# Performance work log

Measured on AMD Instinct MI355X. Metric: run time of the kernel, lower is better.

Reference implementation:

```python
import jax, jax.numpy as jnp
import numpy as np
from jax import lax

RATIO = 0.25
K = 16
EPS = 1e-5
B, N, CX, COUT, CAUX = 16, 4096, 64, 128, 32


def _fps(p, m):
    # Farthest point sampling on one cloud p:(N,3); deterministic start at index 0.
    mind = jnp.sum((p - p[0]) ** 2, axis=-1)  # (N,) min sq-dist to selected set
    def step(mind, _):
        nxt = jnp.argmax(mind)
        d = jnp.sum((p - p[nxt]) ** 2, axis=-1)
        return jnp.minimum(mind, d), nxt
    _, rest = lax.scan(step, mind, None, length=m - 1)
    return jnp.concatenate([jnp.zeros((1,), jnp.int32), rest.astype(jnp.int32)])


def setup_inputs() -> dict:
    key = jax.random.key(0)
    k1, k2, k3, k4, k5, k6 = jax.random.split(key, 6)
    P = B * N
    x = jax.random.normal(k1, (P, CX), jnp.float32)
    pos = jax.random.normal(k2, (P, 3), jnp.float32)
    batch = jnp.repeat(jnp.arange(B, dtype=jnp.int32), N)  # equal-size clouds
    aux = jax.random.normal(k3, (P, CAUX), jnp.float32)
    # MLP params: Linear(CX->COUT) + BatchNorm affine
    W = jax.random.normal(k4, (CX, COUT), jnp.float32) * (1.0 / np.sqrt(CX))
    b = jax.random.normal(k5, (COUT,), jnp.float32) * 0.02
    gamma = jnp.ones((COUT,), jnp.float32) + 0.1 * jax.random.normal(k6, (COUT,), jnp.float32)
    beta = jnp.zeros((COUT,), jnp.float32)
    return {"x": x, "pos": pos, "batch": batch, "aux": aux,
            "W": W, "b": b, "gamma": gamma, "beta": beta}


def reference(x, pos, batch, aux, W, b, gamma, beta):
    P = x.shape[0]
    nb = int(batch[-1]) + 1            # number of clouds (equal-size)
    n = P // nb
    m = int(n * RATIO)                 # clusters per cloud
    pos_b = pos.reshape(nb, n, 3)
    # --- FPS per cloud ---
    idx_local = jax.vmap(lambda p: _fps(p, m))(pos_b)                     # (B, M)
    id_clusters = (idx_local + jnp.arange(nb, dtype=jnp.int32)[:, None] * n).reshape(-1)
    centers = jnp.take_along_axis(pos_b, idx_local[..., None], axis=1)    # (B, M, 3)
    # --- kNN of all points to cluster centers, within each cloud ---
    d2 = jnp.sum((centers[:, :, None, :] - pos_b[:, None, :, :]) ** 2, axis=-1)  # (B, M, N)
    _, nb_local = lax.top_k(-d2, K)                                       # (B, M, K)
    nb_global = (nb_local + jnp.arange(nb, dtype=jnp.int32)[:, None, None] * n).reshape(-1)
    # --- MLP: Linear -> BatchNorm(batch stats, train mode) -> ReLU ---
    h = x @ W + b
    mu = jnp.mean(h, axis=0)
    var = jnp.var(h, axis=0)
    x_trans = jax.nn.relu(gamma * (h - mu) * lax.rsqrt(var + EPS) + beta)  # (P, Cout)
    # --- gather + per-cluster max / mean pooling (== scatter over knn edges) ---
    x_out = jnp.max(x_trans[nb_global].reshape(nb * m, K, -1), axis=1)     # (B*M, Cout)
    aux_out = jnp.mean(aux[nb_global].reshape(nb * m, K, -1), axis=1)      # (B*M, Caux)
    sub_pos = centers.reshape(-1, 3)
    sub_batch = batch[id_clusters]
    return x_out, sub_pos, sub_batch, aux_out, id_clusters
```

## Files before the change

kernel.cpp:

```cpp
#include <hip/hip_runtime.h>
#include <hip/hip_bf16.h>
#include <math.h>

#define NB    16
#define NPC   4096
#define MPC   1024
#define PTOT  65536
#define NCLU  16384
#define KNN_  16
#define CIN   64
#define COUT_ 128
#define CAUX_ 32

#define OFF_XOUT   0
#define OFF_SUBPOS (NCLU*COUT_)
#define OFF_SUBB   (OFF_SUBPOS + NCLU*3)
#define OFF_AUX    (OFF_SUBB + NCLU)
#define OFF_IDCL   (OFF_AUX + NCLU*CAUX_)

#define WS_H        0
#define WS_CENTERS  (PTOT*COUT_*4)
#define WS_STATS    (WS_CENTERS + NCLU*16)
#define WS_NEED     (WS_STATS + 256*4)

#define SM_LX    0
#define SM_LY    16384
#define SM_LZ    32768
#define SM_CAND  49152
#define SM_CSEL  49664
#define SM_XT    0
#define SM_WL    17408
#define SM_BS    50176
#define SM_BQ    50688
#define SM_SIZE  53760

__device__ __forceinline__ double dmax(double a, double b) { return __builtin_fmax(a, b); }
__device__ __forceinline__ double dmin(double a, double b) { return __builtin_fmin(a, b); }
__device__ __forceinline__ double pk(float d, int lo) {
  return __hiloint2double(__float_as_int(d), lo);
}
__device__ __forceinline__ int pk_lo(double k) {
  return (int)(unsigned)(__double_as_longlong(k) & 0xFFFFFFFFll);
}

template <int CTRL>
__device__ __forceinline__ double dpp64(double v) {
  long long u = __double_as_longlong(v);
  int lo = (int)(unsigned)(u & 0xFFFFFFFFll);
  int hi = (int)(unsigned)((unsigned long long)u >> 32);
  int rlo = __builtin_amdgcn_update_dpp(0, lo, CTRL, 0xf, 0xf, true);
  int rhi = __builtin_amdgcn_update_dpp(0, hi, CTRL, 0xf, 0xf, true);
  return __longlong_as_double(((long long)rhi << 32) | (long long)(unsigned)rlo);
}
#define ROR1 0x121
#define ROR2 0x122
#define ROR4 0x124
#define ROR8 0x128

__device__ __forceinline__ double rowmax16(double w) {
  w = dmax(w, dpp64<ROR1>(w));
  w = dmax(w, dpp64<ROR2>(w));
  w = dmax(w, dpp64<ROR4>(w));
  w = dmax(w, dpp64<ROR8>(w));
  return w;
}

__device__ void fps_block(char* smem, const float* __restrict__ pos,
                          float4* __restrict__ centers, float* __restrict__ out)
{
  #pragma clang fp contract(off)
  float* lx = (float*)(smem + SM_LX);
  float* ly = (float*)(smem + SM_LY);
  float* lz = (float*)(smem + SM_LZ);
  double* cand = (double*)(smem + SM_CAND);
  int*   csel = (int*)(smem + SM_CSEL);
  const int b = blockIdx.x;
  const int t = threadIdx.x;
  const float* pb = pos + (size_t)b * NPC * 3;
  const int entry  = (t >> 6) * 4 + ((t >> 4) & 3);
  const bool writer = ((t & 15) == 0);

  float px[8], py[8], pz[8], mind[8];
  int lo8[8];
  {
    const float4* src = (const float4*)(pb + t * 24);
    float4 v[6];
    #pragma unroll
    for (int i = 0; i < 6; ++i) v[i] = src[i];
    const float* f = (const float*)v;
    #pragma unroll
    for (int j = 0; j < 8; ++j) {
      px[j] = f[3*j]; py[j] = f[3*j+1]; pz[j] = f[3*j+2];
      lx[t*8+j] = px[j]; ly[t*8+j] = py[j]; lz[t*8+j] = pz[j];
      lo8[j] = 4095 - (t*8 + j);
    }
  }
  __syncthreads();
  const float x0 = lx[0], y0 = ly[0], z0 = lz[0];
  if (t == 0) csel[0] = 0;

  double bk;
  {
    double k4[4];
    #pragma unroll
    for (int jp = 0; jp < 4; ++jp) {
      const int j0 = 2*jp, j1 = 2*jp + 1;
      float dx0 = px[j0]-x0, dy0 = py[j0]-y0, dz0 = pz[j0]-z0;
      float dx1 = px[j1]-x0, dy1 = py[j1]-y0, dz1 = pz[j1]-z0;
      float d0 = (dx0*dx0 + dy0*dy0) + dz0*dz0;
      float d1 = (dx1*dx1 + dy1*dy1) + dz1*dz1;
      mind[j0] = d0; mind[j1] = d1;
      k4[jp] = dmax(pk(d0, lo8[j0]), pk(d1, lo8[j1]));
    }
    bk = dmax(dmax(k4[0], k4[1]), dmax(k4[2], k4[3]));
  }

  for (int s = 1; s < MPC; ++s) {
    double w = rowmax16(bk);
    const int ph = (s & 1) * 32;
    if (writer) cand[ph + entry] = w;
    __syncthreads();
    double2 pr = ((const double2*)(cand + ph))[t & 15];
    double w2 = rowmax16(dmax(pr.x, pr.y));
    const int sel = 4095 - pk_lo(w2);
    const float sx = lx[sel], sy = ly[sel], sz = lz[sel];
    if (t == 0) csel[s] = sel;
    double k4[4];
    #pragma unroll
    for (int jp = 0; jp < 4; ++jp) {
      const int j0 = 2*jp, j1 = 2*jp + 1;
      float dx0 = px[j0]-sx, dy0 = py[j0]-sy, dz0 = pz[j0]-sz;
      float dx1 = px[j1]-sx, dy1 = py[j1]-sy, dz1 = pz[j1]-sz;
      float d0 = (dx0*dx0 + dy0*dy0) + dz0*dz0;
      float d1 = (dx1*dx1 + dy1*dy1) + dz1*dz1;
      float m0 = fminf(mind[j0], d0), m1 = fminf(mind[j1], d1);
      mind[j0] = m0; mind[j1] = m1;
      k4[jp] = dmax(pk(m0, lo8[j0]), pk(m1, lo8[j1]));
    }
    bk = dmax(dmax(k4[0], k4[1]), dmax(k4[2], k4[3]));
  }
  __syncthreads();
  for (int c = t; c < MPC; c += 512) {
    const int il = csel[c];
    const int cl = b*MPC + c;
    const float X = lx[il], Y = ly[il], Z = lz[il];
    centers[cl] = make_float4(X, Y, Z, 0.0f);
    out[OFF_SUBPOS + cl*3 + 0] = X;
    out[OFF_SUBPOS + cl*3 + 1] = Y;
    out[OFF_SUBPOS + cl*3 + 2] = Z;
    out[OFF_SUBB + cl] = (float)b;
    out[OFF_IDCL + cl] = (float)(b*NPC + il);
  }
}

__device__ void gemm_block(char* smem, const float* __restrict__ x,
                           const float* __restrict__ W, const float* __restrict__ bias,
                           float* __restrict__ h, float* __restrict__ stats, int blk)
{
  float (*xT)[68]  = (float(*)[68])(smem + SM_XT);
  float (*Wl)[128] = (float(*)[128])(smem + SM_WL);
  float* bsum = (float*)(smem + SM_BS);
  float* bsq  = (float*)(smem + SM_BQ);
  const int t = threadIdx.x;
  const int row0 = blk * 64;
  if (t < 128) { bsum[t] = 0.0f; bsq[t] = 0.0f; }
  #pragma unroll
  for (int i = 0; i < 8; ++i) {
    const int idx = t + i*512;
    xT[idx & 63][idx >> 6] = x[(size_t)row0*64 + idx];
  }
  #pragma unroll
  for (int i = 0; i < 16; ++i) {
    const int idx = t + i*512;
    ((float*)Wl)[idx] = W[idx];
  }
  __syncthreads();
  const int tx = t & 31, ty = t >> 5;
  float acc[4][4] = {};
  #pragma unroll 8
  for (int k = 0; k < 64; ++k) {
    const float4 a  = *(const float4*)&xT[k][ty*4];
    const float4 b0 = *(const float4*)&Wl[k][tx*4];
    const float av[4] = {a.x, a.y, a.z, a.w};
    const float bw[4] = {b0.x, b0.y, b0.z, b0.w};
    #pragma unroll
    for (int i2 = 0; i2 < 4; ++i2)
      #pragma unroll
      for (int e = 0; e < 4; ++e)
        acc[i2][e] += av[i2] * bw[e];
  }
  const int c0 = tx*4;
  float bb[4];
  #pragma unroll
  for (int e = 0; e < 4; ++e) bb[e] = bias[c0+e];
  float s4[4] = {}, q4[4] = {};
  #pragma unroll
  for (int i2 = 0; i2 < 4; ++i2) {
    float vv[4];
    #pragma unroll
    for (int e = 0; e < 4; ++e) {
      float v = acc[i2][e] + bb[e];
      vv[e] = v; s4[e] += v; q4[e] += v*v;
    }
    const int r = row0 + ty*4 + i2;
    *(float4*)&h[(size_t)r*128 + c0] = make_float4(vv[0], vv[1], vv[2], vv[3]);
  }
  #pragma unroll
  for (int e = 0; e < 4; ++e) {
    atomicAdd(&bsum[c0+e], s4[e]);
    atomicAdd(&bsq[c0+e],  q4[e]);
  }
  __syncthreads();
  if (t < 128) {
    atomicAdd(&stats[t],      bsum[t]);
    atomicAdd(&stats[128+t],  bsq[t]);
  }
}

__global__ __launch_bounds__(512) void fused_fps_gemm(const float* __restrict__ pos,
                                                      float4* __restrict__ centers,
                                                      float* __restrict__ out,
                                                      const float* __restrict__ x,
                                                      const float* __restrict__ W,
                                                      const float* __restrict__ bias,
                                                      float* __restrict__ h,
                                                      float* __restrict__ stats)
{
  __shared__ __align__(16) char smem[SM_SIZE];
  if (blockIdx.x < NB) fps_block(smem, pos, centers, out);
  else                 gemm_block(smem, x, W, bias, h, stats, blockIdx.x - NB);
}

#define KBIG __hiloint2double(0x7f7fffff, 0xffffffff)
#define CD_STRIDE 17

__global__ __launch_bounds__(256) void knn_pool(const float* __restrict__ pos,
                                                const float4* __restrict__ centers,
                                                const float* __restrict__ h,
                                                const float* __restrict__ aux,
                                                const float* __restrict__ stats,
                                                const float* __restrict__ gamma,
                                                const float* __restrict__ beta,
                                                float* __restrict__ out)
{
  #pragma clang fp contract(off)
  __shared__ float4 lp[NPC];
  __shared__ float  scl[128], ssh[128];
  __shared__ int    fid[32][16];
  const int blk = blockIdx.x;
  const int b   = blk >> 5;
  const int c0  = (blk & 31) * 32;
  const int t   = threadIdx.x;
  const int q   = t & 7;
  const int cc  = t >> 3;
  if (t < 128) {
    const float inv = 1.0f / 65536.0f;
    const float mu  = stats[t] * inv;
    const float var = stats[128+t] * inv - mu*mu;
    const float sc  = gamma[t] * rsqrtf(var + 1e-5f);
    scl[t] = sc;
    ssh[t] = beta[t] - mu*sc;
  }
  const float* pb = pos + (size_t)b * NPC * 3;
  for (int i = t; i < NPC; i += 256)
    lp[i] = make_float4(pb[3*i], pb[3*i+1], pb[3*i+2], 0.0f);
  __syncthreads();
  const int cg = b*MPC + c0 + cc;
  const float4 C = centers[cg];
  double L[16];
  #pragma unroll
  for (int k = 0; k < 16; ++k) L[k] = KBIG;
  for (int jj = 0; jj < NPC/8; ++jj) {
    const int j = jj*8 + q;
    const float4 p = lp[j];
    float dx = C.x - p.x, dy = C.y - p.y, dz = C.z - p.z;
    float d2 = (dx*dx + dy*dy) + dz*dz;
    double nk = pk(d2, j);
    if (nk < L[0]) {
      #pragma unroll
      for (int k = 0; k < 15; ++k) L[k] = dmin(L[k], dmax(L[k+1], nk));
      L[15] = dmin(L[15], nk);
    }
  }
  __syncthreads();
  double* cd = (double*)lp;
  #pragma unroll
  for (int k = 0; k < 16; ++k) cd[t*CD_STRIDE + k] = L[k];
  __syncthreads();
  if (q == 0) {
    double M[16];
    #pragma unroll
    for (int k = 0; k < 16; ++k) M[k] = KBIG;
    for (int ss = 0; ss < 8; ++ss) {
      const double* src = cd + (cc*8 + ss)*CD_STRIDE;
      #pragma unroll
      for (int k = 0; k < 16; ++k) {
        double nk = src[k];
        if (nk < M[0]) {
          #pragma unroll
          for (int m = 0; m < 15; ++m) M[m] = dmin(M[m], dmax(M[m+1], nk));
          M[15] = dmin(M[15], nk);
        }
      }
    }
    #pragma unroll
    for (int k = 0; k < 16; ++k) fid[cc][k] = b*NPC + pk_lo(M[k]);
  }
  __syncthreads();
  for (int g = 0; g < 16; ++g) {
    const int cc2 = g*2 + (t >> 7);
    const int col = t & 127;
    const int cl  = b*MPC + c0 + cc2;
    const float sc = scl[col], sh = ssh[col];
    float mv = 0.0f;
    #pragma unroll
    for (int k = 0; k < 16; ++k) {
      const float hv = h[(size_t)fid[cc2][k]*128 + col];
      mv = fmaxf(mv, fmaxf(sc*hv + sh, 0.0f));
    }
    out[OFF_XOUT + (size_t)cl*128 + col] = mv;
    if (col < 32) {
      float s = 0.0f;
      #pragma unroll
      for (int k = 0; k < 16; ++k) s += aux[(size_t)fid[cc2][k]*32 + col];
      out[OFF_AUX + (size_t)cl*32 + col] = s * (1.0f/16.0f);
    }
  }
}

extern "C" void kernel_launch(void* const* d_in, const int* in_sizes, int n_in,
                              void* d_out, int out_size, void* d_ws, size_t ws_size,
                              hipStream_t stream)
{
  const float* x     = (const float*)d_in[0];
  const float* pos   = (const float*)d_in[1];
  const float* aux   = (const float*)d_in[3];
  const float* W     = (const float*)d_in[4];
  const float* bias  = (const float*)d_in[5];
  const float* gamma = (const float*)d_in[6];
  const float* beta  = (const float*)d_in[7];
  float* out = (float*)d_out;
  char*  ws  = (char*)d_ws;
  if (ws_size < (size_t)WS_NEED) return;

  float*  h       = (float*)(ws + WS_H);
  float4* centers = (float4*)(ws + WS_CENTERS);
  float*  stats   = (float*)(ws + WS_STATS);

  hipMemsetAsync(stats, 0, 256*4, stream);
  hipLaunchKernelGGL(fused_fps_gemm, dim3(NB + PTOT/64), dim3(512), 0, stream,
                     pos, centers, out, x, W, bias, h, stats);
  hipLaunchKernelGGL(knn_pool, dim3(512), dim3(256), 0, stream,
                     pos, centers, h, aux, stats, gamma, beta, out);
}
```

Measured before the change: 762.2 us.

## Process two FPS clouds per block to share barrier cost

Each FPS block now runs farthest-point sampling for two clouds at once, interleaving their distance updates and reductions so that one __syncthreads per step serves both clouds. The aim is to hide the per-iteration barrier and DPP reduction latency, which dominate the serial 1023-step loop, behind twice the independent work. In exchange, register pressure doubles and shared memory per block grows to about 105 KB, which also applies to the GEMM blocks in the same fused kernel and may lower their occupancy. The grid drops to 8 FPS blocks.

```diff
diff --git a/kernel.cpp b/kernel.cpp
--- a/kernel.cpp
+++ b/kernel.cpp
@@ -23,16 +23,21 @@
 #define WS_STATS    (WS_CENTERS + NCLU*16)
 #define WS_NEED     (WS_STATS + 256*4)
 
-#define SM_LX    0
-#define SM_LY    16384
-#define SM_LZ    32768
-#define SM_CAND  49152
-#define SM_CSEL  49664
+#define SM_LXA   0
+#define SM_LYA   16384
+#define SM_LZA   32768
+#define SM_LXB   49152
+#define SM_LYB   65536
+#define SM_LZB   81920
+#define SM_CANDA 98304
+#define SM_CANDB 98816
+#define SM_CSELA 99328
+#define SM_CSELB 103424
 #define SM_XT    0
 #define SM_WL    17408
 #define SM_BS    50176
 #define SM_BQ    50688
-#define SM_SIZE  53760
+#define SM_SIZE  107520
 
 __device__ __forceinline__ double dmax(double a, double b) { return __builtin_fmax(a, b); }
 __device__ __forceinline__ double dmin(double a, double b) { return __builtin_fmin(a, b); }
@@ -65,91 +70,136 @@
   return w;
 }
 
-__device__ void fps_block(char* smem, const float* __restrict__ pos,
-                          float4* __restrict__ centers, float* __restrict__ out)
+__device__ void fps_block2(char* smem, const float* __restrict__ pos,
+                           float4* __restrict__ centers, float* __restrict__ out,
+                           int b0)
 {
   #pragma clang fp contract(off)
-  float* lx = (float*)(smem + SM_LX);
-  float* ly = (float*)(smem + SM_LY);
-  float* lz = (float*)(smem + SM_LZ);
-  double* cand = (double*)(smem + SM_CAND);
-  int*   csel = (int*)(smem + SM_CSEL);
-  const int b = blockIdx.x;
+  float* lxA = (float*)(smem + SM_LXA);
+  float* lyA = (float*)(smem + SM_LYA);
+  float* lzA = (float*)(smem + SM_LZA);
+  float* lxB = (float*)(smem + SM_LXB);
+  float* lyB = (float*)(smem + SM_LYB);
+  float* lzB = (float*)(smem + SM_LZB);
+  double* candA = (double*)(smem + SM_CANDA);
+  double* candB = (double*)(smem + SM_CANDB);
+  int* cselA = (int*)(smem + SM_CSELA);
+  int* cselB = (int*)(smem + SM_CSELB);
   const int t = threadIdx.x;
-  const float* pb = pos + (size_t)b * NPC * 3;
+  const float* pbA = pos + (size_t)b0 * NPC * 3;
+  const float* pbB = pos + (size_t)(b0+1) * NPC * 3;
   const int entry  = (t >> 6) * 4 + ((t >> 4) & 3);
   const bool writer = ((t & 15) == 0);
 
-  float px[8], py[8], pz[8], mind[8];
+  float pxA[8], pyA[8], pzA[8], mindA[8];
+  float pxB[8], pyB[8], pzB[8], mindB[8];
   int lo8[8];
   {
-    const float4* src = (const float4*)(pb + t * 24);
-    float4 v[6];
-    #pragma unroll
-    for (int i = 0; i < 6; ++i) v[i] = src[i];
-    const float* f = (const float*)v;
+    const float4* srcA = (const float4*)(pbA + t * 24);
+    const float4* srcB = (const float4*)(pbB + t * 24);
+    float4 vA[6], vB[6];
+    #pragma unroll
+    for (int i = 0; i < 6; ++i) { vA[i] = srcA[i]; vB[i] = srcB[i]; }
+    const float* fA = (const float*)vA;
+    const float* fB = (const float*)vB;
     #pragma unroll
     for (int j = 0; j < 8; ++j) {
-      px[j] = f[3*j]; py[j] = f[3*j+1]; pz[j] = f[3*j+2];
-      lx[t*8+j] = px[j]; ly[t*8+j] = py[j]; lz[t*8+j] = pz[j];
+      pxA[j] = fA[3*j]; pyA[j] = fA[3*j+1]; pzA[j] = fA[3*j+2];
+      pxB[j] = fB[3*j]; pyB[j] = fB[3*j+1]; pzB[j] = fB[3*j+2];
+      lxA[t*8+j] = pxA[j]; lyA[t*8+j] = pyA[j]; lzA[t*8+j] = pzA[j];
+      lxB[t*8+j] = pxB[j]; lyB[t*8+j] = pyB[j]; lzB[t*8+j] = pzB[j];
       lo8[j] = 4095 - (t*8 + j);
     }
   }
   __syncthreads();
-  const float x0 = lx[0], y0 = ly[0], z0 = lz[0];
-  if (t == 0) csel[0] = 0;
-
-  double bk;
+  const float x0A = lxA[0], y0A = lyA[0], z0A = lzA[0];
+  const float x0B = lxB[0], y0B = lyB[0], z0B = lzB[0];
+  if (t == 0) { cselA[0] = 0; cselB[0] = 0; }
+
+  double bkA, bkB;
   {
-    double k4[4];
+    double kA[4], kB[4];
     #pragma unroll
     for (int jp = 0; jp < 4; ++jp) {
       const int j0 = 2*jp, j1 = 2*jp + 1;
-      float dx0 = px[j0]-x0, dy0 = py[j0]-y0, dz0 = pz[j0]-z0;
-      float dx1 = px[j1]-x0, dy1 = py[j1]-y0, dz1 = pz[j1]-z0;
-      float d0 = (dx0*dx0 + dy0*dy0) + dz0*dz0;
-      float d1 = (dx1*dx1 + dy1*dy1) + dz1*dz1;
-      mind[j0] = d0; mind[j1] = d1;
-      k4[jp] = dmax(pk(d0, lo8[j0]), pk(d1, lo8[j1]));
-    }
-    bk = dmax(dmax(k4[0], k4[1]), dmax(k4[2], k4[3]));
+      float axd0 = pxA[j0]-x0A, ayd0 = pyA[j0]-y0A, azd0 = pzA[j0]-z0A;
+      float axd1 = pxA[j1]-x0A, ayd1 = pyA[j1]-y0A, azd1 = pzA[j1]-z0A;
+      float bxd0 = pxB[j0]-x0B, byd0 = pyB[j0]-y0B, bzd0 = pzB[j0]-z0B;
+      float bxd1 = pxB[j1]-x0B, byd1 = pyB[j1]-y0B, bzd1 = pzB[j1]-z0B;
+      float dA0 = (axd0*axd0 + ayd0*ayd0) + azd0*azd0;
+      float dA1 = (axd1*axd1 + ayd1*ayd1) + azd1*azd1;
+      float dB0 = (bxd0*bxd0 + byd0*byd0) + bzd0*bzd0;
+      float dB1 = (bxd1*bxd1 + byd1*byd1) + bzd1*bzd1;
+      mindA[j0] = dA0; mindA[j1] = dA1;
+      mindB[j0] = dB0; mindB[j1] = dB1;
+      kA[jp] = dmax(pk(dA0, lo8[j0]), pk(dA1, lo8[j1]));
+      kB[jp] = dmax(pk(dB0, lo8[j0]), pk(dB1, lo8[j1]));
+    }
+    bkA = dmax(dmax(kA[0], kA[1]), dmax(kA[2], kA[3]));
+    bkB = dmax(dmax(kB[0], kB[1]), dmax(kB[2], kB[3]));
   }
 
   for (int s = 1; s < MPC; ++s) {
-    double w = rowmax16(bk);
+    double wA = rowmax16(bkA);
+    double wB = rowmax16(bkB);
     const int ph = (s & 1) * 32;
-    if (writer) cand[ph + entry] = w;
+    if (writer) { candA[ph + entry] = wA; candB[ph + entry] = wB; }
     __syncthreads();
-    double2 pr = ((const double2*)(cand + ph))[t & 15];
-    double w2 = rowmax16(dmax(pr.x, pr.y));
-    const int sel = 4095 - pk_lo(w2);
-    const float sx = lx[sel], sy = ly[sel], sz = lz[sel];
-    if (t == 0) csel[s] = sel;
-    double k4[4];
+    double2 prA = ((const double2*)(candA + ph))[t & 15];
+    double2 prB = ((const double2*)(candB + ph))[t & 15];
+    double wA2 = rowmax16(dmax(prA.x, prA.y));
+    double wB2 = rowmax16(dmax(prB.x, prB.y));
+    const int selA = 4095 - pk_lo(wA2);
+    const int selB = 4095 - pk_lo(wB2);
+    const float sxA = lxA[selA], syA = lyA[selA], szA = lzA[selA];
+    const float sxB = lxB[selB], syB = lyB[selB], szB = lzB[selB];
+    if (t == 0) { cselA[s] = selA; cselB[s] = selB; }
+    double kA[4], kB[4];
     #pragma unroll
     for (int jp = 0; jp < 4; ++jp) {
       const int j0 = 2*jp, j1 = 2*jp + 1;
-      float dx0 = px[j0]-sx, dy0 = py[j0]-sy, dz0 = pz[j0]-sz;
-      float dx1 = px[j1]-sx, dy1 = py[j1]-sy, dz1 = pz[j1]-sz;
-      float d0 = (dx0*dx0 + dy0*dy0) + dz0*dz0;
-      float d1 = (dx1*dx1 + dy1*dy1) + dz1*dz1;
-      float m0 = fminf(mind[j0], d0), m1 = fminf(mind[j1], d1);
-      mind[j0] = m0; mind[j1] = m1;
-      k4[jp] = dmax(pk(m0, lo8[j0]), pk(m1, lo8[j1]));
-    }
-    bk = dmax(dmax(k4[0], k4[1]), dmax(k4[2], k4[3]));
+      float axd0 = pxA[j0]-sxA, ayd0 = pyA[j0]-syA, azd0 = pzA[j0]-szA;
+      float axd1 = pxA[j1]-sxA, ayd1 = pyA[j1]-syA, azd1 = pzA[j1]-szA;
+      float bxd0 = pxB[j0]-sxB, byd0 = pyB[j0]-syB, bzd0 = pzB[j0]-szB;
+      float bxd1 = pxB[j1]-sxB, byd1 = pyB[j1]-syB, bzd1 = pzB[j1]-szB;
+      float dA0 = (axd0*axd0 + ayd0*ayd0) + azd0*azd0;
+      float dA1 = (axd1*axd1 + ayd1*ayd1) + azd1*azd1;
+      float dB0 = (bxd0*bxd0 + byd0*byd0) + bzd0*bzd0;
+      float dB1 = (bxd1*bxd1 + byd1*byd1) + bzd1*bzd1;
+      float mA0 = fminf(mindA[j0], dA0), mA1 = fminf(mindA[j1], dA1);
+      float mB0 = fminf(mindB[j0], dB0), mB1 = fminf(mindB[j1], dB1);
+      mindA[j0] = mA0; mindA[j1] = mA1;
+      mindB[j0] = mB0; mindB[j1] = mB1;
+      kA[jp] = dmax(pk(mA0, lo8[j0]), pk(mA1, lo8[j1]));
+      kB[jp] = dmax(pk(mB0, lo8[j0]), pk(mB1, lo8[j1]));
+    }
+    bkA = dmax(dmax(kA[0], kA[1]), dmax(kA[2], kA[3]));
+    bkB = dmax(dmax(kB[0], kB[1]), dmax(kB[2], kB[3]));
   }
   __syncthreads();
   for (int c = t; c < MPC; c += 512) {
-    const int il = csel[c];
-    const int cl = b*MPC + c;
-    const float X = lx[il], Y = ly[il], Z = lz[il];
-    centers[cl] = make_float4(X, Y, Z, 0.0f);
-    out[OFF_SUBPOS + cl*3 + 0] = X;
-    out[OFF_SUBPOS + cl*3 + 1] = Y;
-    out[OFF_SUBPOS + cl*3 + 2] = Z;
-    out[OFF_SUBB + cl] = (float)b;
-    out[OFF_IDCL + cl] = (float)(b*NPC + il);
+    {
+      const int il = cselA[c];
+      const int cl = b0*MPC + c;
+      const float X = lxA[il], Y = lyA[il], Z = lzA[il];
+      centers[cl] = make_float4(X, Y, Z, 0.0f);
+      out[OFF_SUBPOS + cl*3 + 0] = X;
+      out[OFF_SUBPOS + cl*3 + 1] = Y;
+      out[OFF_SUBPOS + cl*3 + 2] = Z;
+      out[OFF_SUBB + cl] = (float)b0;
+      out[OFF_IDCL + cl] = (float)(b0*NPC + il);
+    }
+    {
+      const int il = cselB[c];
+      const int cl = (b0+1)*MPC + c;
+      const float X = lxB[il], Y = lyB[il], Z = lzB[il];
+      centers[cl] = make_float4(X, Y, Z, 0.0f);
+      out[OFF_SUBPOS + cl*3 + 0] = X;
+      out[OFF_SUBPOS + cl*3 + 1] = Y;
+      out[OFF_SUBPOS + cl*3 + 2] = Z;
+      out[OFF_SUBB + cl] = (float)(b0+1);
+      out[OFF_IDCL + cl] = (float)((b0+1)*NPC + il);
+    }
   }
 }
 
@@ -227,8 +277,8 @@
                                                       float* __restrict__ stats)
 {
   __shared__ __align__(16) char smem[SM_SIZE];
-  if (blockIdx.x < NB) fps_block(smem, pos, centers, out);
-  else                 gemm_block(smem, x, W, bias, h, stats, blockIdx.x - NB);
+  if (blockIdx.x < NB/2) fps_block2(smem, pos, centers, out, blockIdx.x * 2);
+  else                   gemm_block(smem, x, W, bias, h, stats, blockIdx.x - NB/2);
 }
 
 #define KBIG __hiloint2double(0x7f7fffff, 0xffffffff)
@@ -348,7 +398,7 @@
   float*  stats   = (float*)(ws + WS_STATS);
 
   hipMemsetAsync(stats, 0, 256*4, stream);
-  hipLaunchKernelGGL(fused_fps_gemm, dim3(NB + PTOT/64), dim3(512), 0, stream,
+  hipLaunchKernelGGL(fused_fps_gemm, dim3(NB/2 + PTOT/64), dim3(512), 0, stream,
                      pos, centers, out, x, W, bias, h, stats);
   hipLaunchKernelGGL(knn_pool, dim3(512), dim3(256), 0, stream,
                      pos, centers, h, aux, stats, gamma, beta, out);
```

New measurement: 1.199 ms. 57.3% more time.

## Split kNN scan across 16 lanes per center with tree merge of candidate lists

Applied to the files above, without the earlier changes.

The knn_pool kernel now uses 512 threads per block, with 16 lanes per cluster center instead of 8. Each lane scans 256 points instead of 512. The per-lane top-16 lists are merged in two stages of 4-way merges rather than one serial 8-way merge. Block indices are also permuted so that consecutive blocks spread across clouds. The aim is to shorten the serial insertion scan and raise parallelism, at the cost of more LDS (a larger candidate buffer) and lower occupancy per CU.

```diff
diff --git a/kernel.cpp b/kernel.cpp
--- a/kernel.cpp
+++ b/kernel.cpp
@@ -234,7 +234,13 @@
 #define KBIG __hiloint2double(0x7f7fffff, 0xffffffff)
 #define CD_STRIDE 17
 
-__global__ __launch_bounds__(256) void knn_pool(const float* __restrict__ pos,
+#define KP_CD    0
+#define KP_SCL   69632
+#define KP_SSH   70144
+#define KP_FID   70656
+#define KP_SIZE  72704
+
+__global__ __launch_bounds__(512) void knn_pool(const float* __restrict__ pos,
                                                 const float4* __restrict__ centers,
                                                 const float* __restrict__ h,
                                                 const float* __restrict__ aux,
@@ -244,15 +250,18 @@
                                                 float* __restrict__ out)
 {
   #pragma clang fp contract(off)
-  __shared__ float4 lp[NPC];
-  __shared__ float  scl[128], ssh[128];
-  __shared__ int    fid[32][16];
-  const int blk = blockIdx.x;
-  const int b   = blk >> 5;
-  const int c0  = (blk & 31) * 32;
+  __shared__ __align__(16) char sm2[KP_SIZE];
+  float4* lp = (float4*)(sm2);
+  double* cd = (double*)(sm2 + KP_CD);
+  float*  scl = (float*)(sm2 + KP_SCL);
+  float*  ssh = (float*)(sm2 + KP_SSH);
+  int*    fid = (int*)(sm2 + KP_FID);
+  const int vblk = ((blockIdx.x & 7) << 6) | (blockIdx.x >> 3);
+  const int b   = vblk >> 5;
+  const int c0  = (vblk & 31) * 32;
   const int t   = threadIdx.x;
-  const int q   = t & 7;
-  const int cc  = t >> 3;
+  const int q   = t & 15;
+  const int cc  = t >> 4;
   if (t < 128) {
     const float inv = 1.0f / 65536.0f;
     const float mu  = stats[t] * inv;
@@ -262,16 +271,15 @@
     ssh[t] = beta[t] - mu*sc;
   }
   const float* pb = pos + (size_t)b * NPC * 3;
-  for (int i = t; i < NPC; i += 256)
+  for (int i = t; i < NPC; i += 512)
     lp[i] = make_float4(pb[3*i], pb[3*i+1], pb[3*i+2], 0.0f);
   __syncthreads();
-  const int cg = b*MPC + c0 + cc;
-  const float4 C = centers[cg];
+  const float4 C = centers[b*MPC + c0 + cc];
   double L[16];
   #pragma unroll
   for (int k = 0; k < 16; ++k) L[k] = KBIG;
-  for (int jj = 0; jj < NPC/8; ++jj) {
-    const int j = jj*8 + q;
+  for (int jj = 0; jj < NPC/16; ++jj) {
+    const int j = jj*16 + q;
     const float4 p = lp[j];
     float dx = C.x - p.x, dy = C.y - p.y, dz = C.z - p.z;
     float d2 = (dx*dx + dy*dy) + dz*dz;
@@ -283,46 +291,61 @@
     }
   }
   __syncthreads();
-  double* cd = (double*)lp;
   #pragma unroll
   for (int k = 0; k < 16; ++k) cd[t*CD_STRIDE + k] = L[k];
   __syncthreads();
-  if (q == 0) {
-    double M[16];
-    #pragma unroll
-    for (int k = 0; k < 16; ++k) M[k] = KBIG;
-    for (int ss = 0; ss < 8; ++ss) {
-      const double* src = cd + (cc*8 + ss)*CD_STRIDE;
+  if (q < 4) {
+    #pragma unroll
+    for (int r = 1; r <= 3; ++r) {
+      const double* src = cd + (cc*16 + q + 4*r)*CD_STRIDE;
       #pragma unroll
       for (int k = 0; k < 16; ++k) {
         double nk = src[k];
-        if (nk < M[0]) {
+        if (nk < L[0]) {
           #pragma unroll
-          for (int m = 0; m < 15; ++m) M[m] = dmin(M[m], dmax(M[m+1], nk));
-          M[15] = dmin(M[15], nk);
+          for (int m = 0; m < 15; ++m) L[m] = dmin(L[m], dmax(L[m+1], nk));
+          L[15] = dmin(L[15], nk);
         }
       }
     }
     #pragma unroll
-    for (int k = 0; k < 16; ++k) fid[cc][k] = b*NPC + pk_lo(M[k]);
-  }
-  __syncthreads();
-  for (int g = 0; g < 16; ++g) {
-    const int cc2 = g*2 + (t >> 7);
+    for (int k = 0; k < 16; ++k) cd[t*CD_STRIDE + k] = L[k];
+  }
+  __syncthreads();
+  if (q == 0) {
+    #pragma unroll
+    for (int r = 1; r <= 3; ++r) {
+      const double* src = cd + (cc*16 + r)*CD_STRIDE;
+      #pragma unroll
+      for (int k = 0; k < 16; ++k) {
+        double nk = src[k];
+        if (nk < L[0]) {
+          #pragma unroll
+          for (int m = 0; m < 15; ++m) L[m] = dmin(L[m], dmax(L[m+1], nk));
+          L[15] = dmin(L[15], nk);
+        }
+      }
+    }
+    #pragma unroll
+    for (int k = 0; k < 16; ++k) fid[cc*16 + k] = b*NPC + pk_lo(L[k]);
+  }
+  __syncthreads();
+  for (int g = 0; g < 8; ++g) {
+    const int cc2 = g*4 + (t >> 7);
     const int col = t & 127;
     const int cl  = b*MPC + c0 + cc2;
     const float sc = scl[col], sh = ssh[col];
     float mv = 0.0f;
     #pragma unroll
     for (int k = 0; k < 16; ++k) {
-      const float hv = h[(size_t)fid[cc2][k]*128 + col];
+      const float hv = h[(size_t)fid[cc2*16 + k]*128 + col];
       mv = fmaxf(mv, fmaxf(sc*hv + sh, 0.0f));
     }
     out[OFF_XOUT + (size_t)cl*128 + col] = mv;
     if (col < 32) {
       float s = 0.0f;
       #pragma unroll
-      for (int k = 0; k < 16; ++k) s += aux[(size_t)fid[cc2][k]*32 + col];
+      for (int k = 0; k < 16; ++k) s += aux[(size_t)fid[cc2*16 + k]*32 + col];
       out[OFF_AUX + (size_t)cl*32 + col] = s * (1.0f/16.0f);
     }
   }
@@ -350,6 +373,6 @@
   hipMemsetAsync(stats, 0, 256*4, stream);
   hipLaunchKernelGGL(fused_fps_gemm, dim3(NB + PTOT/64), dim3(512), 0, stream,
                      pos, centers, out, x, W, bias, h, stats);
-  hipLaunchKernelGGL(knn_pool, dim3(512), dim3(256), 0, stream,
+  hipLaunchKernelGGL(knn_pool, dim3(512), dim3(512), 0, stream,
                      pos, centers, h, aux, stats, gamma, beta, out);
 }
```

After: 743.4 us. -2.5%, faster.
